# Optimization experiments

Hardware: AMD Instinct MI355X
Metric: run time of the kernel (lower is better)

## Reference

```python
import jax, jax.numpy as jnp
import numpy as np

T, B, I, H = 512, 64, 512, 256  # H = hidden_size // 2 (per direction)


def setup_inputs() -> dict:
    key = jax.random.key(0)
    ks = jax.random.split(key, 12)
    s = 1.0 / np.sqrt(H)  # torch GRUCell reset_parameters: U(-1/sqrt(H), 1/sqrt(H))
    u = lambda k, shp: jax.random.uniform(k, shp, jnp.float32, -s, s)
    return {
        "seq_input": jax.random.normal(ks[0], (T, B, I), jnp.float32),
        "seq_mask": (jax.random.uniform(ks[1], (T, B)) < 0.9).astype(jnp.float32),
        "W_ih_1": u(ks[2], (3 * H, I)), "W_hh_1": u(ks[3], (3 * H, H)),
        "b_ih_1": u(ks[4], (3 * H,)), "b_hh_1": u(ks[5], (3 * H,)),
        "W_ih_2": u(ks[6], (3 * H, I)), "W_hh_2": u(ks[7], (3 * H, H)),
        "b_ih_2": u(ks[8], (3 * H,)), "b_hh_2": u(ks[9], (3 * H,)),
    }


def _gru_cell(x, h, W_ih, W_hh, b_ih, b_hh):
    # PyTorch GRUCell math (gate order r, z, n)
    gi = x @ W_ih.T + b_ih  # [B, 3H]
    gh = h @ W_hh.T + b_hh  # [B, 3H]
    i_r, i_z, i_n = jnp.split(gi, 3, axis=-1)
    h_r, h_z, h_n = jnp.split(gh, 3, axis=-1)
    r = jax.nn.sigmoid(i_r + h_r)
    z = jax.nn.sigmoid(i_z + h_z)
    n = jnp.tanh(i_n + r * h_n)
    return (1.0 - z) * n + z * h


def _scan_dir(seq_x, seq_m, W_ih, W_hh, b_ih, b_hh):
    h0 = jnp.zeros((seq_x.shape[1], W_hh.shape[1]), seq_x.dtype)
    def step(h, xm):
        x, m = xm
        ht = _gru_cell(x, h, W_ih, W_hh, b_ih, b_hh)
        m = m[:, None]  # [B,1] broadcast over H
        h_new = ht * m + h * (1.0 - m)
        return h_new, ht * m  # original appends hidden_t * mask_t
    hT, outs = jax.lax.scan(step, h0, (seq_x, seq_m))
    return outs, hT  # outs: [T, B, H]


def reference(seq_input, seq_mask, W_ih_1, W_hh_1, b_ih_1, b_hh_1,
              W_ih_2, W_hh_2, b_ih_2, b_hh_2):
    # forward direction
    out1, h1 = _scan_dir(seq_input, seq_mask, W_ih_1, W_hh_1, b_ih_1, b_hh_1)
    # backward direction: scan over reversed time, then re-reverse outputs
    out2_rev, h2 = _scan_dir(seq_input[::-1], seq_mask[::-1], W_ih_2, W_hh_2, b_ih_2, b_hh_2)
    out2 = out2_rev[::-1]
    outputs = jnp.concatenate([out1, out2], axis=-1)  # [T, B, 2H]
    hidden = jnp.stack([h1, h2], axis=0)  # [2, B, H]
    return outputs, hidden
```

## Files before the change

kernel.cpp:

```cpp
#include <hip/hip_runtime.h>
#include <cstdint>

typedef _Float16 half2_t __attribute__((ext_vector_type(2)));
typedef _Float16 half8_t __attribute__((ext_vector_type(8)));
typedef float    floatx4 __attribute__((ext_vector_type(4)));

#define OFF_BIAS  0ull
#define SZ_BIAS   (1536ull*4)
#define OFF_GI    6144ull

__global__ void k_prep(const float* __restrict__ bih1, const float* __restrict__ bih2,
                       const float* __restrict__ bhh1, const float* __restrict__ bhh2,
                       float* __restrict__ biascat) {
    int q3 = blockIdx.x * 256 + threadIdx.x;
    if (q3 < 1536) {
        int dir = q3 >= 768;  int j = q3 - dir*768;
        const float* bi = dir ? bih2 : bih1;
        const float* bh = dir ? bhh2 : bhh1;
        biascat[q3] = bi[j] + (j < 512 ? bh[j] : 0.f);
    }
}

__device__ __forceinline__ half8_t cvt8(float4 a, float4 b) {
    half8_t r;
    r[0] = (_Float16)a.x; r[1] = (_Float16)a.y; r[2] = (_Float16)a.z; r[3] = (_Float16)a.w;
    r[4] = (_Float16)b.x; r[5] = (_Float16)b.y; r[6] = (_Float16)b.z; r[7] = (_Float16)b.w;
    return r;
}

__global__ __launch_bounds__(256) void k_gemm(const float* __restrict__ x,
                                              const float* __restrict__ Wih1,
                                              const float* __restrict__ Wih2,
                                              const float* __restrict__ bias,
                                              _Float16* __restrict__ gi) {
    __shared__ __align__(16) _Float16 As[128*32];
    __shared__ __align__(16) _Float16 Bs[256*32];
    const int tid = threadIdx.x;
    const int m0 = blockIdx.x * 128;
    const int n0 = blockIdx.y * 256;
    const int lane = tid & 63, wave = tid >> 6;
    const int wr = wave >> 1, wc = wave & 1;
    floatx4 acc[4][8];
#pragma unroll
    for (int i = 0; i < 4; ++i)
#pragma unroll
        for (int j = 0; j < 8; ++j) acc[i][j] = (floatx4)0.f;

    const float* Wsrc = (n0 < 768) ? Wih1 : Wih2;
    const int nl = (n0 < 768) ? n0 : (n0 - 768);
    const int ar = tid >> 1, ah = (tid & 1) * 16;
    const float* Ag = x + (size_t)(m0 + ar)*512 + ah;
    const float* Bg = Wsrc + (size_t)(nl + tid)*512;
    _Float16* Aw = As + ar*32 + ah;
    _Float16* Bw = Bs + tid*32;
    const int aoff = (wr*64  + (lane & 15))*32 + (lane >> 4)*8;
    const int boff = (wc*128 + (lane & 15))*32 + (lane >> 4)*8;

    for (int kt = 0; kt < 16; ++kt) {
        const int ko = kt*32;
        float4 a0 = *(const float4*)(Ag + ko);
        float4 a1 = *(const float4*)(Ag + ko + 4);
        float4 a2 = *(const float4*)(Ag + ko + 8);
        float4 a3 = *(const float4*)(Ag + ko + 12);
        float4 b0 = *(const float4*)(Bg + ko);
        float4 b1 = *(const float4*)(Bg + ko + 4);
        float4 b2 = *(const float4*)(Bg + ko + 8);
        float4 b3 = *(const float4*)(Bg + ko + 12);
        float4 b4 = *(const float4*)(Bg + ko + 16);
        float4 b5 = *(const float4*)(Bg + ko + 20);
        float4 b6 = *(const float4*)(Bg + ko + 24);
        float4 b7 = *(const float4*)(Bg + ko + 28);
        __syncthreads();
        *(half8_t*)(Aw)      = cvt8(a0, a1);
        *(half8_t*)(Aw + 8)  = cvt8(a2, a3);
        *(half8_t*)(Bw)      = cvt8(b0, b1);
        *(half8_t*)(Bw + 8)  = cvt8(b2, b3);
        *(half8_t*)(Bw + 16) = cvt8(b4, b5);
        *(half8_t*)(Bw + 24) = cvt8(b6, b7);
        __syncthreads();
        half8_t af[4], bf[8];
#pragma unroll
        for (int f = 0; f < 4; ++f) af[f] = *(const half8_t*)(As + aoff + f*512);
#pragma unroll
        for (int f = 0; f < 8; ++f) bf[f] = *(const half8_t*)(Bs + boff + f*512);
#pragma unroll
        for (int i = 0; i < 4; ++i)
#pragma unroll
            for (int j = 0; j < 8; ++j)
                acc[i][j] = __builtin_amdgcn_mfma_f32_16x16x32_f16(af[i], bf[j], acc[i][j], 0, 0, 0);
    }
#pragma unroll
    for (int i = 0; i < 4; ++i) {
#pragma unroll
        for (int j = 0; j < 8; ++j) {
            int col = n0 + wc*128 + j*16 + (lane & 15);
            float bv = bias[col];
            int dir = col >= 768;
            size_t gib = (size_t)dir * 25165824ull + (size_t)(col - dir*768);
#pragma unroll
            for (int q = 0; q < 4; ++q) {
                int row = m0 + wr*64 + i*16 + (lane >> 4)*4 + q;
                gi[gib + (size_t)row*768] = (_Float16)(acc[i][j][q] + bv);
            }
        }
    }
}

#define FDOT2(w_, h_, acc_) __builtin_amdgcn_fdot2(__builtin_bit_cast(half2_t,(w_)), (h_), (acc_), false)
#define LBAR()  do { asm volatile("s_waitcnt lgkmcnt(0)" ::: "memory"); \
                     __builtin_amdgcn_s_barrier(); } while (0)

__global__ __launch_bounds__(512, 1) void k_rnn(const float* __restrict__ Whh1,
                                                const float* __restrict__ Whh2,
                                                const _Float16* __restrict__ gi,
                                                const float* __restrict__ mask,
                                                const float* __restrict__ bhh1,
                                                const float* __restrict__ bhh2,
                                                float* __restrict__ outp) {
    __shared__ __align__(16) _Float16 hs16[256];
    __shared__ float part[768];
    const int tid = threadIdx.x;
    const int bid = blockIdx.x;
    const int dir = bid >> 6, b = bid & 63;
    const int c  = tid & 255;
    const int kh = tid >> 8;

    const float* W = dir ? Whh2 : Whh1;
    unsigned int w[192];
#pragma unroll
    for (int a = 0; a < 3; ++a) {
        const float* wrow = W + (size_t)(c + a*256)*256 + kh*128;
#pragma unroll
        for (int qq = 0; qq < 64; ++qq) {
            float2 f = *(const float2*)(wrow + 2*qq);
            half2_t hp = {(_Float16)f.x, (_Float16)f.y};
            w[a*64 + qq] = __builtin_bit_cast(unsigned int, hp);
        }
    }
    const float bhn = (dir ? bhh2 : bhh1)[512 + c];

    if (tid < 256) hs16[tid] = (_Float16)0.f;
    float h_c = 0.f;
    __syncthreads();

    const _Float16* gb = gi + (size_t)dir * 25165824ull + c;
    const _Float16* hrd = hs16 + (kh << 7);

#pragma unroll 1
    for (int s = 0; s < 512; ++s) {
        const int t = dir ? (511 - s) : s;
        float g0 = 0.f, g1 = 0.f, g2 = 0.f, mv = 0.f;
        if (tid < 256) {
            const _Float16* gp = gb + (size_t)(t*64 + b)*768;
            g0 = (float)gp[0];
            g1 = (float)gp[256];
            g2 = (float)gp[512];
            mv = mask[t*64 + b];
        }
        float a0 = 0.f, a1 = 0.f, a2 = 0.f;
        float b0 = 0.f, b1 = 0.f, b2 = 0.f;
#pragma unroll
        for (int kk = 0; kk < 16; ++kk) {
            half8_t hv = *(const half8_t*)(hrd + (kk << 3));
            half2_t h0 = {hv[0], hv[1]};
            half2_t h1 = {hv[2], hv[3]};
            half2_t h2 = {hv[4], hv[5]};
            half2_t h3 = {hv[6], hv[7]};
            const int q = kk << 2;
            a0 = FDOT2(w[      q + 0], h0, a0);  b0 = FDOT2(w[      q + 1], h1, b0);
            a0 = FDOT2(w[      q + 2], h2, a0);  b0 = FDOT2(w[      q + 3], h3, b0);
            a1 = FDOT2(w[ 64 + q + 0], h0, a1);  b1 = FDOT2(w[ 64 + q + 1], h1, b1);
            a1 = FDOT2(w[ 64 + q + 2], h2, a1);  b1 = FDOT2(w[ 64 + q + 3], h3, b1);
            a2 = FDOT2(w[128 + q + 0], h0, a2);  b2 = FDOT2(w[128 + q + 1], h1, b2);
            a2 = FDOT2(w[128 + q + 2], h2, a2);  b2 = FDOT2(w[128 + q + 3], h3, b2);
        }
        a0 += b0; a1 += b1; a2 += b2;
        if (tid >= 256) { part[c] = a0; part[256 + c] = a1; part[512 + c] = a2; }
        LBAR();
        if (tid < 256) {
            float ghr = a0 + part[c];
            float ghz = a1 + part[256 + c];
            float ghn = a2 + part[512 + c];
            float r = 1.f / (1.f + __expf(-(g0 + ghr)));
            float z = 1.f / (1.f + __expf(-(g1 + ghz)));
            float tt = g2 + r * (ghn + bhn);
            float ea = __expf(-2.f * fabsf(tt));
            float nt = (1.f - ea) / (1.f + ea);
            nt = (tt < 0.f) ? -nt : nt;
            float ht = (1.f - z) * nt + z * h_c;
            float hm = mv * ht + (1.f - mv) * h_c;
            h_c = hm;
            hs16[c] = (_Float16)hm;
            outp[(size_t)(t*64 + b)*512 + dir*256 + c] = mv * ht;
        }
        LBAR();
    }
    if (tid < 256) {
        outp[16777216u + dir*16384 + b*256 + c] = h_c;
    }
}

extern "C" void kernel_launch(void* const* d_in, const int* in_sizes, int n_in,
                              void* d_out, int out_size, void* d_ws, size_t ws_size,
                              hipStream_t stream) {
    const float* x    = (const float*)d_in[0];
    const float* mask = (const float*)d_in[1];
    const float* Wih1 = (const float*)d_in[2];
    const float* Whh1 = (const float*)d_in[3];
    const float* bih1 = (const float*)d_in[4];
    const float* bhh1 = (const float*)d_in[5];
    const float* Wih2 = (const float*)d_in[6];
    const float* Whh2 = (const float*)d_in[7];
    const float* bih2 = (const float*)d_in[8];
    const float* bhh2 = (const float*)d_in[9];
    char* ws = (char*)d_ws;
    float* biascat = (float*)(ws + OFF_BIAS);
    _Float16* gi   = (_Float16*)(ws + OFF_GI);
    float* outp = (float*)d_out;

    hipLaunchKernelGGL(k_prep, dim3(6), dim3(256), 0, stream,
                       bih1, bih2, bhh1, bhh2, biascat);
    hipLaunchKernelGGL(k_gemm, dim3(256, 6), dim3(256), 0, stream, x, Wih1, Wih2, biascat, gi);
    hipLaunchKernelGGL(k_rnn, dim3(128), dim3(512), 0, stream,
                       Whh1, Whh2, gi, mask, bhh1, bhh2, outp);
}
```

Baseline: 845.4 us.

## Process two batch rows per RNN block to reuse register-resident weights

Each recurrent block now handles two batch elements instead of one, so every register-held W_hh value feeds two dot products. The grid halves from 128 to 64 blocks, and the shared hidden and partial-sum buffers double in size. This aims to amortize barrier and LDS synchronization over more work per step. The cost is more arithmetic and a longer serial gate epilogue per step on fewer CUs.

```diff
diff --git a/kernel.cpp b/kernel.cpp
--- a/kernel.cpp
+++ b/kernel.cpp
@@ -110,18 +110,19 @@
 #define LBAR()  do { asm volatile("s_waitcnt lgkmcnt(0)" ::: "memory"); \
                      __builtin_amdgcn_s_barrier(); } while (0)
 
-__global__ __launch_bounds__(512, 1) void k_rnn(const float* __restrict__ Whh1,
-                                                const float* __restrict__ Whh2,
-                                                const _Float16* __restrict__ gi,
-                                                const float* __restrict__ mask,
-                                                const float* __restrict__ bhh1,
-                                                const float* __restrict__ bhh2,
-                                                float* __restrict__ outp) {
-    __shared__ __align__(16) _Float16 hs16[256];
-    __shared__ float part[768];
+__global__ __launch_bounds__(512) void k_rnn(const float* __restrict__ Whh1,
+                                             const float* __restrict__ Whh2,
+                                             const _Float16* __restrict__ gi,
+                                             const float* __restrict__ mask,
+                                             const float* __restrict__ bhh1,
+                                             const float* __restrict__ bhh2,
+                                             float* __restrict__ outp) {
+    __shared__ __align__(16) _Float16 hs16[512];
+    __shared__ float part[1536];
     const int tid = threadIdx.x;
     const int bid = blockIdx.x;
-    const int dir = bid >> 6, b = bid & 63;
+    const int dir = bid >> 5;
+    const int b0  = (bid & 31) * 2;
     const int c  = tid & 255;
     const int kh = tid >> 8;
 
@@ -139,64 +140,97 @@
     }
     const float bhn = (dir ? bhh2 : bhh1)[512 + c];
 
-    if (tid < 256) hs16[tid] = (_Float16)0.f;
-    float h_c = 0.f;
+    hs16[tid] = (_Float16)0.f;
+    float h_c0 = 0.f, h_c1 = 0.f;
     __syncthreads();
 
     const _Float16* gb = gi + (size_t)dir * 25165824ull + c;
-    const _Float16* hrd = hs16 + (kh << 7);
+    const _Float16* hrd0 = hs16 + (kh << 7);
+    const _Float16* hrd1 = hs16 + 256 + (kh << 7);
 
 #pragma unroll 1
     for (int s = 0; s < 512; ++s) {
         const int t = dir ? (511 - s) : s;
-        float g0 = 0.f, g1 = 0.f, g2 = 0.f, mv = 0.f;
+        float g00 = 0.f, g01 = 0.f, g02 = 0.f, mv0 = 0.f;
+        float g10 = 0.f, g11 = 0.f, g12 = 0.f, mv1 = 0.f;
         if (tid < 256) {
-            const _Float16* gp = gb + (size_t)(t*64 + b)*768;
-            g0 = (float)gp[0];
-            g1 = (float)gp[256];
-            g2 = (float)gp[512];
-            mv = mask[t*64 + b];
-        }
-        float a0 = 0.f, a1 = 0.f, a2 = 0.f;
-        float b0 = 0.f, b1 = 0.f, b2 = 0.f;
+            const _Float16* gp = gb + (size_t)(t*64 + b0)*768;
+            g00 = (float)gp[0];    g01 = (float)gp[256];       g02 = (float)gp[512];
+            g10 = (float)gp[768];  g11 = (float)gp[768+256];   g12 = (float)gp[768+512];
+            mv0 = mask[t*64 + b0];
+            mv1 = mask[t*64 + b0 + 1];
+        }
+        float x0 = 0.f, x1 = 0.f, x2 = 0.f;
+        float y0 = 0.f, y1 = 0.f, y2 = 0.f;
+        float u0 = 0.f, u1 = 0.f, u2 = 0.f;
+        float v0 = 0.f, v1 = 0.f, v2 = 0.f;
 #pragma unroll
         for (int kk = 0; kk < 16; ++kk) {
-            half8_t hv = *(const half8_t*)(hrd + (kk << 3));
-            half2_t h0 = {hv[0], hv[1]};
-            half2_t h1 = {hv[2], hv[3]};
-            half2_t h2 = {hv[4], hv[5]};
-            half2_t h3 = {hv[6], hv[7]};
+            half8_t ha = *(const half8_t*)(hrd0 + (kk << 3));
+            half8_t hb = *(const half8_t*)(hrd1 + (kk << 3));
+            half2_t a0p = {ha[0], ha[1]}, a1p = {ha[2], ha[3]};
+            half2_t a2p = {ha[4], ha[5]}, a3p = {ha[6], ha[7]};
+            half2_t b0p = {hb[0], hb[1]}, b1p = {hb[2], hb[3]};
+            half2_t b2p = {hb[4], hb[5]}, b3p = {hb[6], hb[7]};
             const int q = kk << 2;
-            a0 = FDOT2(w[      q + 0], h0, a0);  b0 = FDOT2(w[      q + 1], h1, b0);
-            a0 = FDOT2(w[      q + 2], h2, a0);  b0 = FDOT2(w[      q + 3], h3, b0);
-            a1 = FDOT2(w[ 64 + q + 0], h0, a1);  b1 = FDOT2(w[ 64 + q + 1], h1, b1);
-            a1 = FDOT2(w[ 64 + q + 2], h2, a1);  b1 = FDOT2(w[ 64 + q + 3], h3, b1);
-            a2 = FDOT2(w[128 + q + 0], h0, a2);  b2 = FDOT2(w[128 + q + 1], h1, b2);
-            a2 = FDOT2(w[128 + q + 2], h2, a2);  b2 = FDOT2(w[128 + q + 3], h3, b2);
-        }
-        a0 += b0; a1 += b1; a2 += b2;
-        if (tid >= 256) { part[c] = a0; part[256 + c] = a1; part[512 + c] = a2; }
+            unsigned int w0 = w[q+0], w1 = w[q+1], w2 = w[q+2], w3 = w[q+3];
+            x0 = FDOT2(w0, a0p, x0);  u0 = FDOT2(w0, b0p, u0);
+            y0 = FDOT2(w1, a1p, y0);  v0 = FDOT2(w1, b1p, v0);
+            x0 = FDOT2(w2, a2p, x0);  u0 = FDOT2(w2, b2p, u0);
+            y0 = FDOT2(w3, a3p, y0);  v0 = FDOT2(w3, b3p, v0);
+            unsigned int z0 = w[64+q+0], z1 = w[64+q+1], z2 = w[64+q+2], z3 = w[64+q+3];
+            x1 = FDOT2(z0, a0p, x1);  u1 = FDOT2(z0, b0p, u1);
+            y1 = FDOT2(z1, a1p, y1);  v1 = FDOT2(z1, b1p, v1);
+            x1 = FDOT2(z2, a2p, x1);  u1 = FDOT2(z2, b2p, u1);
+            y1 = FDOT2(z3, a3p, y1);  v1 = FDOT2(z3, b3p, v1);
+            unsigned int n0 = w[128+q+0], n1 = w[128+q+1], n2 = w[128+q+2], n3 = w[128+q+3];
+            x2 = FDOT2(n0, a0p, x2);  u2 = FDOT2(n0, b0p, u2);
+            y2 = FDOT2(n1, a1p, y2);  v2 = FDOT2(n1, b1p, v2);
+            x2 = FDOT2(n2, a2p, x2);  u2 = FDOT2(n2, b2p, u2);
+            y2 = FDOT2(n3, a3p, y2);  v2 = FDOT2(n3, b3p, v2);
+        }
+        x0 += y0; x1 += y1; x2 += y2;
+        u0 += v0; u1 += v1; u2 += v2;
+        if (tid >= 256) {
+            part[c]        = x0; part[256 + c]  = x1; part[512 + c]  = x2;
+            part[768 + c]  = u0; part[1024 + c] = u1; part[1280 + c] = u2;
+        }
         LBAR();
         if (tid < 256) {
-            float ghr = a0 + part[c];
-            float ghz = a1 + part[256 + c];
-            float ghn = a2 + part[512 + c];
-            float r = 1.f / (1.f + __expf(-(g0 + ghr)));
-            float z = 1.f / (1.f + __expf(-(g1 + ghz)));
-            float tt = g2 + r * (ghn + bhn);
+            float ghr = x0 + part[c];
+            float ghz = x1 + part[256 + c];
+            float ghn = x2 + part[512 + c];
+            float r = 1.f / (1.f + __expf(-(g00 + ghr)));
+            float z = 1.f / (1.f + __expf(-(g01 + ghz)));
+            float tt = g02 + r * (ghn + bhn);
             float ea = __expf(-2.f * fabsf(tt));
             float nt = (1.f - ea) / (1.f + ea);
             nt = (tt < 0.f) ? -nt : nt;
-            float ht = (1.f - z) * nt + z * h_c;
-            float hm = mv * ht + (1.f - mv) * h_c;
-            h_c = hm;
+            float ht = (1.f - z) * nt + z * h_c0;
+            float hm = mv0 * ht + (1.f - mv0) * h_c0;
+            h_c0 = hm;
             hs16[c] = (_Float16)hm;
-            outp[(size_t)(t*64 + b)*512 + dir*256 + c] = mv * ht;
+            outp[(size_t)(t*64 + b0)*512 + dir*256 + c] = mv0 * ht;
+            ghr = u0 + part[768 + c];
+            ghz = u1 + part[1024 + c];
+            ghn = u2 + part[1280 + c];
+            r = 1.f / (1.f + __expf(-(g10 + ghr)));
+            z = 1.f / (1.f + __expf(-(g11 + ghz)));
+            tt = g12 + r * (ghn + bhn);
+            ea = __expf(-2.f * fabsf(tt));
+            nt = (1.f - ea) / (1.f + ea);
+            nt = (tt < 0.f) ? -nt : nt;
+            ht = (1.f - z) * nt + z * h_c1;
+            hm = mv1 * ht + (1.f - mv1) * h_c1;
+            h_c1 = hm;
+            hs16[256 + c] = (_Float16)hm;
+            outp[(size_t)(t*64 + b0 + 1)*512 + dir*256 + c] = mv1 * ht;
         }
         LBAR();
     }
     if (tid < 256) {
-        outp[16777216u + dir*16384 + b*256 + c] = h_c;
+        outp[16777216u + dir*16384 + b0*256 + c]       = h_c0;
+        outp[16777216u + dir*16384 + (b0+1)*256 + c]   = h_c1;
     }
 }
 
@@ -221,6 +255,6 @@
     hipLaunchKernelGGL(k_prep, dim3(6), dim3(256), 0, stream,
                        bih1, bih2, bhh1, bhh2, biascat);
     hipLaunchKernelGGL(k_gemm, dim3(256, 6), dim3(256), 0, stream, x, Wih1, Wih2, biascat, gi);
-    hipLaunchKernelGGL(k_rnn, dim3(128), dim3(512), 0, stream,
+    hipLaunchKernelGGL(k_rnn, dim3(64), dim3(512), 0, stream,
                        Whh1, Whh2, gi, mask, bhh1, bhh2, outp);
 }
```

Result: slower. 1.288 ms (+52.3%).
